# Performance work log

Measured on AMD Instinct MI355X. Metric: run time of the kernel, lower is better.

## Reference

```python
import jax, jax.numpy as jnp
import numpy as np

USER_NUM = 100000
ITEM_NUM = 100000
N = USER_NUM + ITEM_NUM
D = 64
N_EDGES = 3200000
N_LAYERS = 3
LAYER_CL = 1
EPS = 0.2


def setup_inputs() -> dict:
    key = jax.random.key(0)
    k1, k2, k3, k4, k5, k6 = jax.random.split(key, 6)
    user_emb = jax.random.normal(k1, (USER_NUM, D), dtype=jnp.float32)
    item_emb = jax.random.normal(k2, (ITEM_NUM, D), dtype=jnp.float32)
    adj_src = jax.random.randint(k3, (N_EDGES,), 0, N, dtype=jnp.int64)
    adj_dst = jax.random.randint(k4, (N_EDGES,), 0, N, dtype=jnp.int64)
    adj_vals = jax.random.uniform(k5, (N_EDGES,), dtype=jnp.float32)
    noise = jax.random.uniform(k6, (N_LAYERS, N, D), dtype=jnp.float32)
    return {"user_emb": user_emb, "item_emb": item_emb, "adj_src": adj_src,
            "adj_dst": adj_dst, "adj_vals": adj_vals, "noise": noise}


def reference(user_emb, item_emb, adj_src, adj_dst, adj_vals, noise):
    # ego_embeddings = cat([user_emb, item_emb])  -> [N, D]
    ego = jnp.concatenate([user_emb, item_emb], axis=0)
    acc = jnp.zeros_like(ego)
    cl = ego
    for k in range(N_LAYERS):
        # sparse.mm: out[dst] += val * ego[src]
        msg = ego[adj_src] * adj_vals[:, None]          # [E, D]
        ego = jax.ops.segment_sum(msg, adj_dst, num_segments=N)
        # perturbed noise injection: ego += sign(ego) * F.normalize(noise, dim=-1) * eps
        rn = noise[k]
        rn = rn / jnp.maximum(jnp.linalg.norm(rn, axis=-1, keepdims=True), 1e-12)
        ego = ego + jnp.sign(ego) * rn * EPS
        acc = acc + ego
        if k == LAYER_CL - 1:
            cl = ego
    final = acc / N_LAYERS  # mean over stacked layer outputs
    return (final[:USER_NUM], final[USER_NUM:], cl[:USER_NUM], cl[USER_NUM:])
```

## Files before the change

kernel.cpp:

```cpp
#include <hip/hip_runtime.h>

#define USER_NUM 100000
#define ITEM_NUM 100000
#define NN 200000
#define DIM 64
#define EPSV 0.2f

#define NB 196
#define BSH 10
#define NPB 1024
#define CH 4096
#define PER 16
#define SRC_MASK 0x3FFFF

__global__ __launch_bounds__(256) void bhist_k(const int* __restrict__ dst,
                                               int* __restrict__ bhist, int E) {
    __shared__ int h[NB];
    int t = threadIdx.x;
    for (int i = t; i < NB; i += 256) h[i] = 0;
    __syncthreads();
    long long base = (long long)blockIdx.x * CH;
    #pragma unroll
    for (int j = 0; j < PER; ++j) {
        long long e = base + t + j * 256;
        if (e < E) atomicAdd(&h[dst[e] >> BSH], 1);
    }
    __syncthreads();
    for (int i = t; i < NB; i += 256) if (h[i]) atomicAdd(&bhist[i], h[i]);
}

__global__ __launch_bounds__(256) void bscan_k(const int* __restrict__ bhist,
                                               int* __restrict__ bucket_base,
                                               int* __restrict__ bucket_off,
                                               int* __restrict__ row_ptr, int E) {
    __shared__ int tmp[256];
    int t = threadIdx.x;
    int s = (t < NB) ? bhist[t] : 0;
    tmp[t] = s;
    __syncthreads();
    for (int off = 1; off < 256; off <<= 1) {
        int x = (t >= off) ? tmp[t - off] : 0;
        __syncthreads();
        tmp[t] += x;
        __syncthreads();
    }
    int excl = tmp[t] - s;
    if (t < NB) { bucket_base[t] = excl; bucket_off[t] = excl; }
    if (t == 0) { bucket_base[NB] = E; row_ptr[NN] = E; }
}

__global__ __launch_bounds__(256) void apart_k(const int* __restrict__ src,
                                               const int* __restrict__ dst,
                                               const float* __restrict__ vals,
                                               int* __restrict__ bucket_off,
                                               int2* __restrict__ out, int E) {
    __shared__ int cnt[NB], start[NB], cursor[NB], gbase[NB];
    __shared__ int tmp[256];
    __shared__ int2 rec[CH];
    int t = threadIdx.x;
    long long base = (long long)blockIdx.x * CH;
    int nvalid = (int)min((long long)CH, (long long)E - base);

    int s_[PER]; int d_[PER]; float v_[PER];
    for (int i = t; i < NB; i += 256) cnt[i] = 0;
    __syncthreads();
    #pragma unroll
    for (int j = 0; j < PER; ++j) {
        int idx = t + j * 256;
        if (idx < nvalid) {
            long long e = base + idx;
            d_[j] = dst[e]; s_[j] = src[e]; v_[j] = vals[e];
            atomicAdd(&cnt[d_[j] >> BSH], 1);
        } else d_[j] = -1;
    }
    __syncthreads();
    int c = (t < NB) ? cnt[t] : 0;
    tmp[t] = c;
    __syncthreads();
    for (int off = 1; off < 256; off <<= 1) {
        int x = (t >= off) ? tmp[t - off] : 0;
        __syncthreads();
        tmp[t] += x;
        __syncthreads();
    }
    if (t < NB) {
        int excl = tmp[t] - c;
        start[t] = excl; cursor[t] = excl;
        gbase[t] = (c > 0) ? atomicAdd(&bucket_off[t], c) : 0;
    }
    __syncthreads();
    #pragma unroll
    for (int j = 0; j < PER; ++j) {
        if (d_[j] >= 0) {
            int b = d_[j] >> BSH;
            int slot = atomicAdd(&cursor[b], 1);
            rec[slot] = make_int2(s_[j] | ((d_[j] & (NPB - 1)) << 18),
                                  __float_as_int(v_[j]));
        }
    }
    __syncthreads();
    for (int slot = t; slot < nvalid; slot += 256) {
        int lo = 0, hi = NB - 1;
        while (lo < hi) {
            int mid = (lo + hi + 1) >> 1;
            if (start[mid] <= slot) lo = mid; else hi = mid - 1;
        }
        out[gbase[lo] + (slot - start[lo])] = rec[slot];
    }
}

__global__ __launch_bounds__(256) void bsort_k(const int* __restrict__ bucket_base,
                                               const int2* __restrict__ in,
                                               int2* __restrict__ out,
                                               int* __restrict__ row_ptr) {
    __shared__ int noff[NPB];
    __shared__ int tmp[256];
    int b = blockIdx.x, t = threadIdx.x;
    int rbeg = bucket_base[b], rend = bucket_base[b + 1];
    for (int i = t; i < NPB; i += 256) noff[i] = 0;
    __syncthreads();
    for (int i = rbeg + t; i < rend; i += 256)
        atomicAdd(&noff[(in[i].x >> 18) & (NPB - 1)], 1);
    __syncthreads();
    int l0 = noff[t * 4], l1 = noff[t * 4 + 1], l2 = noff[t * 4 + 2], l3 = noff[t * 4 + 3];
    int s = l0 + l1 + l2 + l3;
    tmp[t] = s;
    __syncthreads();
    for (int off = 1; off < 256; off <<= 1) {
        int x = (t >= off) ? tmp[t - off] : 0;
        __syncthreads();
        tmp[t] += x;
        __syncthreads();
    }
    int run = rbeg + tmp[t] - s;
    int e0 = run, e1 = run + l0, e2 = e1 + l1, e3 = e2 + l2;
    noff[t * 4] = e0; noff[t * 4 + 1] = e1; noff[t * 4 + 2] = e2; noff[t * 4 + 3] = e3;
    int node0 = b * NPB + t * 4;
    if (node0 < NN)     row_ptr[node0]     = e0;
    if (node0 + 1 < NN) row_ptr[node0 + 1] = e1;
    if (node0 + 2 < NN) row_ptr[node0 + 2] = e2;
    if (node0 + 3 < NN) row_ptr[node0 + 3] = e3;
    __syncthreads();
    for (int i = rbeg + t; i < rend; i += 256) {
        int2 r = in[i];
        int pos = atomicAdd(&noff[(r.x >> 18) & (NPB - 1)], 1);
        out[pos] = r;
    }
}

__device__ __forceinline__ unsigned int bpack(float a, float b) {
    unsigned int ua = __float_as_uint(a), ub = __float_as_uint(b);
    ua = (ua + 0x7fffu + ((ua >> 16) & 1u)) >> 16;
    ub = (ub + 0x7fffu + ((ub >> 16) & 1u)) >> 16;
    return ua | (ub << 16);
}

__device__ __forceinline__ float bsign(float x) {
    return (x > 0.f) ? 1.f : ((x < 0.f) ? -1.f : 0.f);
}

__global__ __launch_bounds__(256) void cvt_k(const float* __restrict__ ue,
                                             const float* __restrict__ ie,
                                             unsigned int* __restrict__ out) {
    long long i = (long long)blockIdx.x * 256 + threadIdx.x;
    const long long tot = (long long)NN * (DIM / 4);
    if (i >= tot) return;
    const long long uu = (long long)USER_NUM * (DIM / 4);
    const float4 v = (i < uu) ? reinterpret_cast<const float4*>(ue)[i]
                              : reinterpret_cast<const float4*>(ie)[i - uu];
    uint2 p; p.x = bpack(v.x, v.y); p.y = bpack(v.z, v.w);
    reinterpret_cast<uint2*>(out)[i] = p;
}

#define FMA8(q, vv)                                                          \
    do {                                                                     \
        float t0 = __uint_as_float((q).x << 16);                             \
        float t1 = __uint_as_float((q).x & 0xffff0000u);                     \
        float t2 = __uint_as_float((q).y << 16);                             \
        float t3 = __uint_as_float((q).y & 0xffff0000u);                     \
        float t4 = __uint_as_float((q).z << 16);                             \
        float t5 = __uint_as_float((q).z & 0xffff0000u);                     \
        float t6 = __uint_as_float((q).w << 16);                             \
        float t7 = __uint_as_float((q).w & 0xffff0000u);                     \
        a0 = fma((double)t0, (vv), a0); a1 = fma((double)t1, (vv), a1);      \
        a2 = fma((double)t2, (vv), a2); a3 = fma((double)t3, (vv), a3);      \
        a4 = fma((double)t4, (vv), a4); a5 = fma((double)t5, (vv), a5);      \
        a6 = fma((double)t6, (vv), a6); a7 = fma((double)t7, (vv), a7);      \
    } while (0)

__global__ __launch_bounds__(256) void spmm_fused_k(const int* __restrict__ row_ptr,
                                                    const int2* __restrict__ ssv,
                                                    const unsigned int* __restrict__ ego,
                                                    unsigned int* __restrict__ ego_out,
                                                    float* __restrict__ cl_out,
                                                    const float* __restrict__ nz_layer,
                                                    float* __restrict__ acc,
                                                    int is_first, int is_last) {
    int node = blockIdx.x * 4 + (threadIdx.x >> 6);
    int lane = threadIdx.x & 63;
    int g    = lane >> 3;
    int d8   = lane & 7;
    int beg = row_ptr[node];
    int end = row_ptr[node + 1];

    double a0 = 0, a1 = 0, a2 = 0, a3 = 0, a4 = 0, a5 = 0, a6 = 0, a7 = 0;
    int base = beg;

    for (; base + 16 <= end; base += 16) {
        int2 svA = ssv[base + g];
        int2 svB = ssv[base + 8 + g];
        int sA = svA.x & SRC_MASK;
        int sB = svB.x & SRC_MASK;
        const uint4 qA = *reinterpret_cast<const uint4*>(ego + ((size_t)sA << 5) + (d8 << 2));
        const uint4 qB = *reinterpret_cast<const uint4*>(ego + ((size_t)sB << 5) + (d8 << 2));
        double vA = (double)__int_as_float(svA.y);
        double vB = (double)__int_as_float(svB.y);
        FMA8(qA, vA);
        FMA8(qB, vB);
    }
    if (base + 8 <= end) {
        int2 sv = ssv[base + g];
        int s = sv.x & SRC_MASK;
        const uint4 q = *reinterpret_cast<const uint4*>(ego + ((size_t)s << 5) + (d8 << 2));
        double v = (double)__int_as_float(sv.y);
        FMA8(q, v);
        base += 8;
    }
    int rem = end - base;
    if (rem > 0) {
        int2 sv = ssv[base + ((g < rem) ? g : 0)];
        int s = sv.x & SRC_MASK;
        const uint4 q = *reinterpret_cast<const uint4*>(ego + ((size_t)s << 5) + (d8 << 2));
        double v = (g < rem) ? (double)__int_as_float(sv.y) : 0.0;
        FMA8(q, v);
    }

    a0 += __shfl_xor(a0, 8, 64);  a1 += __shfl_xor(a1, 8, 64);
    a2 += __shfl_xor(a2, 8, 64);  a3 += __shfl_xor(a3, 8, 64);
    a4 += __shfl_xor(a4, 8, 64);  a5 += __shfl_xor(a5, 8, 64);
    a6 += __shfl_xor(a6, 8, 64);  a7 += __shfl_xor(a7, 8, 64);
    a0 += __shfl_xor(a0, 16, 64); a1 += __shfl_xor(a1, 16, 64);
    a2 += __shfl_xor(a2, 16, 64); a3 += __shfl_xor(a3, 16, 64);
    a4 += __shfl_xor(a4, 16, 64); a5 += __shfl_xor(a5, 16, 64);
    a6 += __shfl_xor(a6, 16, 64); a7 += __shfl_xor(a7, 16, 64);
    a0 += __shfl_xor(a0, 32, 64); a1 += __shfl_xor(a1, 32, 64);
    a2 += __shfl_xor(a2, 32, 64); a3 += __shfl_xor(a3, 32, 64);
    a4 += __shfl_xor(a4, 32, 64); a5 += __shfl_xor(a5, 32, 64);
    a6 += __shfl_xor(a6, 32, 64); a7 += __shfl_xor(a7, 32, 64);

    float f0 = (float)a0, f1 = (float)a1, f2 = (float)a2, f3 = (float)a3;
    float f4 = (float)a4, f5 = (float)a5, f6 = (float)a6, f7 = (float)a7;

    size_t off = (size_t)node * DIM + (d8 << 3);
    const float4 n0 = *reinterpret_cast<const float4*>(nz_layer + off);
    const float4 n1 = *reinterpret_cast<const float4*>(nz_layer + off + 4);
    float ss = n0.x * n0.x + n0.y * n0.y + n0.z * n0.z + n0.w * n0.w
             + n1.x * n1.x + n1.y * n1.y + n1.z * n1.z + n1.w * n1.w;
    ss += __shfl_xor(ss, 1, 64);
    ss += __shfl_xor(ss, 2, 64);
    ss += __shfl_xor(ss, 4, 64);
    float e = EPSV / fmaxf(sqrtf(ss), 1e-12f);

    float w0 = f0 + bsign(f0) * n0.x * e;
    float w1 = f1 + bsign(f1) * n0.y * e;
    float w2 = f2 + bsign(f2) * n0.z * e;
    float w3 = f3 + bsign(f3) * n0.w * e;
    float w4 = f4 + bsign(f4) * n1.x * e;
    float w5 = f5 + bsign(f5) * n1.y * e;
    float w6 = f6 + bsign(f6) * n1.z * e;
    float w7 = f7 + bsign(f7) * n1.w * e;

    if (g == 0) {
        if (!is_last) {
            uint4 p;
            p.x = bpack(w0, w1); p.y = bpack(w2, w3);
            p.z = bpack(w4, w5); p.w = bpack(w6, w7);
            *reinterpret_cast<uint4*>(ego_out + ((size_t)node << 5) + (d8 << 2)) = p;
        }
        float4 v0 = make_float4(w0, w1, w2, w3);
        float4 v1 = make_float4(w4, w5, w6, w7);
        if (cl_out) {
            *reinterpret_cast<float4*>(cl_out + off)     = v0;
            *reinterpret_cast<float4*>(cl_out + off + 4) = v1;
        }
        float4 r0, r1;
        if (is_first) {
            r0 = v0; r1 = v1;
        } else {
            const float4 p0 = *reinterpret_cast<const float4*>(acc + off);
            const float4 p1 = *reinterpret_cast<const float4*>(acc + off + 4);
            r0.x = p0.x + v0.x; r0.y = p0.y + v0.y; r0.z = p0.z + v0.z; r0.w = p0.w + v0.w;
            r1.x = p1.x + v1.x; r1.y = p1.y + v1.y; r1.z = p1.z + v1.z; r1.w = p1.w + v1.w;
        }
        if (is_last) {
            const float k = 1.0f / 3.0f;
            r0.x *= k; r0.y *= k; r0.z *= k; r0.w *= k;
            r1.x *= k; r1.y *= k; r1.z *= k; r1.w *= k;
        }
        *reinterpret_cast<float4*>(acc + off)     = r0;
        *reinterpret_cast<float4*>(acc + off + 4) = r1;
    }
}

extern "C" void kernel_launch(void* const* d_in, const int* in_sizes, int n_in,
                              void* d_out, int out_size, void* d_ws, size_t ws_size,
                              hipStream_t stream) {
    const float* user_emb = (const float*)d_in[0];
    const float* item_emb = (const float*)d_in[1];
    const int*   adj_src  = (const int*)d_in[2];
    const int*   adj_dst  = (const int*)d_in[3];
    const float* adj_vals = (const float*)d_in[4];
    const float* noise    = (const float*)d_in[5];
    const int E = in_sizes[2];

    const long long ND = (long long)NN * DIM;
    float* out_final = (float*)d_out;
    float* out_cl    = out_final + ND;

    char* w = (char*)d_ws;
    const long long B16 = (long long)NN * (DIM / 2) * 4;
    unsigned int* egoB0 = (unsigned int*)w;
    int2*         ssv_b = (int2*)w;
    unsigned int* egoB1 = (unsigned int*)(w + B16);
    int2*         ssv   = (int2*)(w + 2 * B16);
    int*   bhist   = (int*)(w + 3 * B16);
    int*   bbase   = bhist + NB;
    int*   boff    = bbase + NB + 1;
    int*   row_ptr = boff + NB;

    const int nchunk = (E + CH - 1) / CH;

    hipMemsetAsync(bhist, 0, NB * sizeof(int), stream);
    bhist_k<<<nchunk, 256, 0, stream>>>(adj_dst, bhist, E);
    bscan_k<<<1, 256, 0, stream>>>(bhist, bbase, boff, row_ptr, E);
    apart_k<<<nchunk, 256, 0, stream>>>(adj_src, adj_dst, adj_vals, boff, ssv_b, E);
    bsort_k<<<NB, 256, 0, stream>>>(bbase, ssv_b, ssv, row_ptr);
    cvt_k<<<(int)(((long long)NN * (DIM / 4) + 255) / 256), 256, 0, stream>>>(
        user_emb, item_emb, egoB0);

    const int spmm_grid = NN / 4;
    spmm_fused_k<<<spmm_grid, 256, 0, stream>>>(row_ptr, ssv, egoB0, egoB1,
                                                out_cl, noise, out_final, 1, 0);
    spmm_fused_k<<<spmm_grid, 256, 0, stream>>>(row_ptr, ssv, egoB1, egoB0,
                                                nullptr, noise + ND, out_final, 0, 0);
    spmm_fused_k<<<spmm_grid, 256, 0, stream>>>(row_ptr, ssv, egoB0, nullptr,
                                                nullptr, noise + 2 * ND, out_final, 0, 1);
}
```

Before: 746.8 us.

## Replace two-level bucket sort CSR build with global atomic counting sort

Replaces the bucketed partition plus per-bucket local sort with a direct per-node histogram, a three-stage prefix scan into row_ptr, and a scatter that uses a global atomic cursor per destination node. This removes the shared-memory staging and the binary-search scatter of the two-pass approach. In exchange, every edge costs two global atomics on random addresses and writes are uncoalesced. Edge order within a row also becomes nondeterministic.

```diff
diff --git a/kernel.cpp b/kernel.cpp
--- a/kernel.cpp
+++ b/kernel.cpp
@@ -6,145 +6,88 @@
 #define DIM 64
 #define EPSV 0.2f
 
-#define NB 196
-#define BSH 10
-#define NPB 1024
-#define CH 4096
-#define PER 16
+#define NBLK 782
 #define SRC_MASK 0x3FFFF
 
-__global__ __launch_bounds__(256) void bhist_k(const int* __restrict__ dst,
-                                               int* __restrict__ bhist, int E) {
-    __shared__ int h[NB];
-    int t = threadIdx.x;
-    for (int i = t; i < NB; i += 256) h[i] = 0;
+__global__ __launch_bounds__(256) void hist_k(const int* __restrict__ dst,
+                                              int* __restrict__ h, int E) {
+    int e = blockIdx.x * 256 + threadIdx.x;
+    if (e < E) atomicAdd(&h[dst[e]], 1);
+}
+
+__global__ __launch_bounds__(256) void psum_k(const int* __restrict__ h,
+                                              int* __restrict__ bsum) {
+    __shared__ int tmp[256];
+    int b = blockIdx.x, t = threadIdx.x;
+    int i = b * 256 + t;
+    tmp[t] = (i < NN) ? h[i] : 0;
     __syncthreads();
-    long long base = (long long)blockIdx.x * CH;
-    #pragma unroll
-    for (int j = 0; j < PER; ++j) {
-        long long e = base + t + j * 256;
-        if (e < E) atomicAdd(&h[dst[e] >> BSH], 1);
-    }
-    __syncthreads();
-    for (int i = t; i < NB; i += 256) if (h[i]) atomicAdd(&bhist[i], h[i]);
-}
-
-__global__ __launch_bounds__(256) void bscan_k(const int* __restrict__ bhist,
-                                               int* __restrict__ bucket_base,
-                                               int* __restrict__ bucket_off,
-                                               int* __restrict__ row_ptr, int E) {
+    for (int o = 128; o > 0; o >>= 1) {
+        if (t < o) tmp[t] += tmp[t + o];
+        __syncthreads();
+    }
+    if (t == 0) bsum[b] = tmp[0];
+}
+
+__global__ __launch_bounds__(256) void bscan2_k(int* __restrict__ bsum,
+                                                int* __restrict__ row_ptr, int E) {
     __shared__ int tmp[256];
     int t = threadIdx.x;
-    int s = (t < NB) ? bhist[t] : 0;
+    int i0 = 4 * t;
+    int v0 = (i0     < NBLK) ? bsum[i0]     : 0;
+    int v1 = (i0 + 1 < NBLK) ? bsum[i0 + 1] : 0;
+    int v2 = (i0 + 2 < NBLK) ? bsum[i0 + 2] : 0;
+    int v3 = (i0 + 3 < NBLK) ? bsum[i0 + 3] : 0;
+    int s = v0 + v1 + v2 + v3;
     tmp[t] = s;
     __syncthreads();
-    for (int off = 1; off < 256; off <<= 1) {
-        int x = (t >= off) ? tmp[t - off] : 0;
+    for (int o = 1; o < 256; o <<= 1) {
+        int x = (t >= o) ? tmp[t - o] : 0;
         __syncthreads();
         tmp[t] += x;
         __syncthreads();
     }
     int excl = tmp[t] - s;
-    if (t < NB) { bucket_base[t] = excl; bucket_off[t] = excl; }
-    if (t == 0) { bucket_base[NB] = E; row_ptr[NN] = E; }
-}
-
-__global__ __launch_bounds__(256) void apart_k(const int* __restrict__ src,
-                                               const int* __restrict__ dst,
-                                               const float* __restrict__ vals,
-                                               int* __restrict__ bucket_off,
-                                               int2* __restrict__ out, int E) {
-    __shared__ int cnt[NB], start[NB], cursor[NB], gbase[NB];
-    __shared__ int tmp[256];
-    __shared__ int2 rec[CH];
-    int t = threadIdx.x;
-    long long base = (long long)blockIdx.x * CH;
-    int nvalid = (int)min((long long)CH, (long long)E - base);
-
-    int s_[PER]; int d_[PER]; float v_[PER];
-    for (int i = t; i < NB; i += 256) cnt[i] = 0;
-    __syncthreads();
-    #pragma unroll
-    for (int j = 0; j < PER; ++j) {
-        int idx = t + j * 256;
-        if (idx < nvalid) {
-            long long e = base + idx;
-            d_[j] = dst[e]; s_[j] = src[e]; v_[j] = vals[e];
-            atomicAdd(&cnt[d_[j] >> BSH], 1);
-        } else d_[j] = -1;
-    }
-    __syncthreads();
-    int c = (t < NB) ? cnt[t] : 0;
-    tmp[t] = c;
-    __syncthreads();
-    for (int off = 1; off < 256; off <<= 1) {
-        int x = (t >= off) ? tmp[t - off] : 0;
-        __syncthreads();
-        tmp[t] += x;
-        __syncthreads();
-    }
-    if (t < NB) {
-        int excl = tmp[t] - c;
-        start[t] = excl; cursor[t] = excl;
-        gbase[t] = (c > 0) ? atomicAdd(&bucket_off[t], c) : 0;
-    }
-    __syncthreads();
-    #pragma unroll
-    for (int j = 0; j < PER; ++j) {
-        if (d_[j] >= 0) {
-            int b = d_[j] >> BSH;
-            int slot = atomicAdd(&cursor[b], 1);
-            rec[slot] = make_int2(s_[j] | ((d_[j] & (NPB - 1)) << 18),
-                                  __float_as_int(v_[j]));
-        }
-    }
-    __syncthreads();
-    for (int slot = t; slot < nvalid; slot += 256) {
-        int lo = 0, hi = NB - 1;
-        while (lo < hi) {
-            int mid = (lo + hi + 1) >> 1;
-            if (start[mid] <= slot) lo = mid; else hi = mid - 1;
-        }
-        out[gbase[lo] + (slot - start[lo])] = rec[slot];
-    }
-}
-
-__global__ __launch_bounds__(256) void bsort_k(const int* __restrict__ bucket_base,
-                                               const int2* __restrict__ in,
-                                               int2* __restrict__ out,
-                                               int* __restrict__ row_ptr) {
-    __shared__ int noff[NPB];
+    if (i0     < NBLK) bsum[i0]     = excl;
+    if (i0 + 1 < NBLK) bsum[i0 + 1] = excl + v0;
+    if (i0 + 2 < NBLK) bsum[i0 + 2] = excl + v0 + v1;
+    if (i0 + 3 < NBLK) bsum[i0 + 3] = excl + v0 + v1 + v2;
+    if (t == 0) row_ptr[NN] = E;
+}
+
+__global__ __launch_bounds__(256) void rowptr_k(const int* __restrict__ h,
+                                                const int* __restrict__ bsum,
+                                                int* __restrict__ row_ptr,
+                                                int* __restrict__ cursor) {
     __shared__ int tmp[256];
     int b = blockIdx.x, t = threadIdx.x;
-    int rbeg = bucket_base[b], rend = bucket_base[b + 1];
-    for (int i = t; i < NPB; i += 256) noff[i] = 0;
+    int i = b * 256 + t;
+    int v = (i < NN) ? h[i] : 0;
+    tmp[t] = v;
     __syncthreads();
-    for (int i = rbeg + t; i < rend; i += 256)
-        atomicAdd(&noff[(in[i].x >> 18) & (NPB - 1)], 1);
-    __syncthreads();
-    int l0 = noff[t * 4], l1 = noff[t * 4 + 1], l2 = noff[t * 4 + 2], l3 = noff[t * 4 + 3];
-    int s = l0 + l1 + l2 + l3;
-    tmp[t] = s;
-    __syncthreads();
-    for (int off = 1; off < 256; off <<= 1) {
-        int x = (t >= off) ? tmp[t - off] : 0;
+    for (int o = 1; o < 256; o <<= 1) {
+        int x = (t >= o) ? tmp[t - o] : 0;
         __syncthreads();
         tmp[t] += x;
         __syncthreads();
     }
-    int run = rbeg + tmp[t] - s;
-    int e0 = run, e1 = run + l0, e2 = e1 + l1, e3 = e2 + l2;
-    noff[t * 4] = e0; noff[t * 4 + 1] = e1; noff[t * 4 + 2] = e2; noff[t * 4 + 3] = e3;
-    int node0 = b * NPB + t * 4;
-    if (node0 < NN)     row_ptr[node0]     = e0;
-    if (node0 + 1 < NN) row_ptr[node0 + 1] = e1;
-    if (node0 + 2 < NN) row_ptr[node0 + 2] = e2;
-    if (node0 + 3 < NN) row_ptr[node0 + 3] = e3;
-    __syncthreads();
-    for (int i = rbeg + t; i < rend; i += 256) {
-        int2 r = in[i];
-        int pos = atomicAdd(&noff[(r.x >> 18) & (NPB - 1)], 1);
-        out[pos] = r;
+    if (i < NN) {
+        int p = bsum[b] + tmp[t] - v;
+        row_ptr[i] = p;
+        cursor[i] = p;
+    }
+}
+
+__global__ __launch_bounds__(256) void scat_k(const int* __restrict__ src,
+                                              const int* __restrict__ dst,
+                                              const float* __restrict__ vals,
+                                              int* __restrict__ cursor,
+                                              int2* __restrict__ ssv, int E) {
+    int e = blockIdx.x * 256 + threadIdx.x;
+    if (e < E) {
+        int d = dst[e];
+        int pos = atomicAdd(&cursor[d], 1);
+        ssv[pos] = make_int2(src[e], __float_as_int(vals[e]));
     }
 }
 
@@ -320,21 +263,21 @@
     char* w = (char*)d_ws;
     const long long B16 = (long long)NN * (DIM / 2) * 4;
     unsigned int* egoB0 = (unsigned int*)w;
-    int2*         ssv_b = (int2*)w;
+    int*          h      = (int*)w;
+    int*          cursor = (int*)(w + (1 << 20));
     unsigned int* egoB1 = (unsigned int*)(w + B16);
     int2*         ssv   = (int2*)(w + 2 * B16);
-    int*   bhist   = (int*)(w + 3 * B16);
-    int*   bbase   = bhist + NB;
-    int*   boff    = bbase + NB + 1;
-    int*   row_ptr = boff + NB;
-
-    const int nchunk = (E + CH - 1) / CH;
-
-    hipMemsetAsync(bhist, 0, NB * sizeof(int), stream);
-    bhist_k<<<nchunk, 256, 0, stream>>>(adj_dst, bhist, E);
-    bscan_k<<<1, 256, 0, stream>>>(bhist, bbase, boff, row_ptr, E);
-    apart_k<<<nchunk, 256, 0, stream>>>(adj_src, adj_dst, adj_vals, boff, ssv_b, E);
-    bsort_k<<<NB, 256, 0, stream>>>(bbase, ssv_b, ssv, row_ptr);
+    int*   row_ptr = (int*)(w + 3 * B16);
+    int*   bsum    = row_ptr + NN + 1;
+
+    const int egrid = (E + 255) / 256;
+
+    hipMemsetAsync(h, 0, NN * sizeof(int), stream);
+    hist_k<<<egrid, 256, 0, stream>>>(adj_dst, h, E);
+    psum_k<<<NBLK, 256, 0, stream>>>(h, bsum);
+    bscan2_k<<<1, 256, 0, stream>>>(bsum, row_ptr, E);
+    rowptr_k<<<NBLK, 256, 0, stream>>>(h, bsum, row_ptr, cursor);
+    scat_k<<<egrid, 256, 0, stream>>>(adj_src, adj_dst, adj_vals, cursor, ssv, E);
     cvt_k<<<(int)(((long long)NN * (DIM / 4) + 255) / 256), 256, 0, stream>>>(
         user_emb, item_emb, egoB0);
 
```

Result: slower. 1.009 ms (+35.1%).
